# Performance work log

Measured on AMD Instinct MI355X. Metric: run time of the kernel, lower is better.

Reference implementation:

```python
import jax, jax.numpy as jnp
import numpy as np

N_NODES = 9
NEG_SLOPE = 0.2
# static edge list from the module (src, dst) pairs, PyG convention row0=src, row1=dst
_E = np.array([[0,1],[1,0],[0,3],[3,0],[0,5],[5,0],[0,7],[7,0],
               [1,2],[2,1],[3,4],[4,3],[5,6],[6,5],[7,8],[8,7]], dtype=np.int32).T
# GATv2Conv default add_self_loops=True
SRC = jnp.asarray(np.concatenate([_E[0], np.arange(N_NODES, dtype=np.int32)]))
DST = jnp.asarray(np.concatenate([_E[1], np.arange(N_NODES, dtype=np.int32)]))


def setup_inputs() -> dict:
    key = jax.random.key(0)
    k1, k2, k3, k4 = jax.random.split(key, 4)
    B, C_IN, C_OUT = 16384, 256, 256
    scale = 1.0 / np.sqrt(C_IN)
    return {
        "x": jax.random.normal(k1, (B, N_NODES, C_IN), jnp.float32),
        "W_l": jax.random.normal(k2, (C_IN, C_OUT), jnp.float32) * scale,
        "W_r": jax.random.normal(k3, (C_IN, C_OUT), jnp.float32) * scale,
        "att": jax.random.normal(k4, (C_OUT,), jnp.float32) * scale,
        "bias": jnp.zeros((C_OUT,), jnp.float32),
    }


def reference(x, W_l, W_r, att, bias):
    # x: [B, N, C_in] batch of identical small graphs
    xl = jnp.einsum("bnc,cd->bnd", x, W_l)  # source-side projection
    xr = jnp.einsum("bnc,cd->bnd", x, W_r)  # target-side projection
    # per-edge GATv2 score: a^T LeakyReLU(x_l[src] + x_r[dst])
    e = jax.nn.leaky_relu(xl[:, SRC] + xr[:, DST], NEG_SLOPE)  # [B, E, C_out]
    score = jnp.einsum("bed,d->be", e, att)                    # [B, E]
    # softmax over incoming edges of each destination node (segment softmax)
    sT = score.T                                               # [E, B]
    m = jax.ops.segment_max(sT, DST, num_segments=N_NODES)     # [N, B]
    ex = jnp.exp(sT - m[DST])
    denom = jax.ops.segment_sum(ex, DST, num_segments=N_NODES)
    alpha = ex / denom[DST]                                    # [E, B]
    # scatter-aggregate messages alpha * x_l[src] into dst
    msg = xl[:, SRC] * alpha.T[..., None]                      # [B, E, C_out]
    out = jax.ops.segment_sum(msg.transpose(1, 0, 2), DST, num_segments=N_NODES)
    return out.transpose(1, 0, 2) + bias                       # [B, N, C_out]
```

## Files before the change

### kernel.cpp

```cpp
#include <hip/hip_runtime.h>
#include <hip/hip_bf16.h>

typedef __attribute__((ext_vector_type(8))) short short8;
typedef __attribute__((ext_vector_type(4))) float f32x4;
typedef __attribute__((ext_vector_type(4))) unsigned short u16x4;

#define XLR_STRIDE 520
#define XLR_BYTES  (144 * XLR_STRIDE * 2)
#define LDS_BYTES  (XLR_BYTES + 1024 + 1600 + 1600)

__device__ __forceinline__ unsigned short f2bf(float f) {
    unsigned int u = __float_as_uint(f);
    unsigned int r = (u + 0x7fffu + ((u >> 16) & 1u)) >> 16;
    return (unsigned short)r;
}
__device__ __forceinline__ float bf2f(unsigned short h) {
    return __uint_as_float(((unsigned int)h) << 16);
}

__device__ const int SRC_E[25] = {0,1,0,3,0,5,0,7,1,2,3,4,5,6,7,8, 0,1,2,3,4,5,6,7,8};
__device__ const int DST_E[25] = {1,0,3,0,5,0,7,0,2,1,4,3,6,5,8,7, 0,1,2,3,4,5,6,7,8};
__device__ const int NINC[9]    = {5,3,2,3,2,3,2,3,2};
__device__ const int INC_OFF[9] = {0,5,8,10,13,15,18,20,23};
__device__ const int INC_E[25]  = {1,3,5,7,16, 0,9,17, 8,18, 2,11,19, 10,20, 4,13,21, 12,22, 6,15,23, 14,24};
__device__ const int INC_S[25]  = {1,3,5,7,0,  0,2,1,  1,2,  0,4,3,   3,4,   0,6,5,   5,6,   0,8,7,   7,8};

__global__ void convert_w_kernel(const float* __restrict__ Wl,
                                 const float* __restrict__ Wr,
                                 unsigned short* __restrict__ WT) {
    int n = blockIdx.x;
    int k = threadIdx.x;
    float v = (n < 256) ? Wl[k * 256 + n] : Wr[k * 256 + (n - 256)];
    WT[n * 256 + k] = f2bf(v);
}

__global__ __launch_bounds__(512, 2) void gat_fused_kernel(
        const float* __restrict__ x,
        const unsigned short* __restrict__ WT,
        const float* __restrict__ att,
        const float* __restrict__ bias,
        float* __restrict__ out) {
    __shared__ __align__(16) char smem[LDS_BYTES];
    unsigned short* XLR = (unsigned short*)smem;
    float* atts   = (float*)(smem + XLR_BYTES);
    float* scores = atts + 256;
    float* alphas = scores + 400;

    const int tid  = threadIdx.x;
    const int lane = tid & 63;
    const int wave = tid >> 6;
    const int blk  = blockIdx.x;

    if (tid < 256) atts[tid] = att[tid];

    const float* xblk = x + (size_t)blk * 36864;
    {
        f32x4 xv[18];
        #pragma unroll
        for (int it = 0; it < 18; ++it)
            xv[it] = *(const f32x4*)(xblk + it * 2048 + tid * 4);
        #pragma unroll
        for (int it = 0; it < 18; ++it) {
            int f   = it * 2048 + tid * 4;
            int row = f >> 8;
            int k   = f & 255;
            int inner = (k * 2) ^ ((row & 15) << 4);
            u16x4 w4 = { f2bf(xv[it][0]), f2bf(xv[it][1]), f2bf(xv[it][2]), f2bf(xv[it][3]) };
            *(u16x4*)(smem + row * 512 + inner) = w4;
        }
    }
    __syncthreads();

    const f32x4 ZERO = {0.f, 0.f, 0.f, 0.f};
    f32x4 acc[9][4];
    #pragma unroll
    for (int m = 0; m < 9; ++m)
        #pragma unroll
        for (int n = 0; n < 4; ++n) acc[m][n] = ZERO;

    const int nb = wave * 64;
    const unsigned short* Wbase = WT + (size_t)((nb + (lane & 15)) * 256 + ((lane >> 4) * 8));
    short8 bnx[4];
    #pragma unroll
    for (int n = 0; n < 4; ++n) bnx[n] = *(const short8*)(Wbase + n * 4096);

    #pragma unroll
    for (int kc = 0; kc < 8; ++kc) {
        short8 bn[4];
        #pragma unroll
        for (int n = 0; n < 4; ++n) bn[n] = bnx[n];
        if (kc < 7) {
            #pragma unroll
            for (int n = 0; n < 4; ++n)
                bnx[n] = *(const short8*)(Wbase + n * 4096 + (kc + 1) * 32);
        }
        short8 am[9];
        const int innerbase = ((kc * 64) + ((lane >> 4) * 16)) ^ ((lane & 15) << 4);
        #pragma unroll
        for (int m = 0; m < 9; ++m) {
            int row = m * 16 + (lane & 15);
            am[m] = *(const short8*)(smem + row * 512 + innerbase);
        }
        #pragma unroll
        for (int m = 0; m < 9; ++m)
            #pragma unroll
            for (int n = 0; n < 4; ++n)
                acc[m][n] = __builtin_amdgcn_mfma_f32_16x16x32_bf16(am[m], bn[n], acc[m][n], 0, 0, 0);
    }
    __syncthreads();

    #pragma unroll
    for (int m = 0; m < 9; ++m) {
        #pragma unroll
        for (int n = 0; n < 4; ++n) {
            int col = nb + n * 16 + (lane & 15);
            #pragma unroll
            for (int r = 0; r < 4; ++r) {
                int row = m * 16 + ((lane >> 4) * 4) + r;
                XLR[row * XLR_STRIDE + col] = f2bf(acc[m][n][r]);
            }
        }
    }
    __syncthreads();

    if (tid < 400) {
        int g = tid / 25, e = tid - g * 25;
        const unsigned short* pl = XLR + (g * 9 + SRC_E[e]) * XLR_STRIDE;
        const unsigned short* pr = XLR + (g * 9 + DST_E[e]) * XLR_STRIDE + 256;
        float s = 0.f;
        #pragma unroll 4
        for (int dc = 0; dc < 32; ++dc) {
            short8 a = *(const short8*)(pl + dc * 8);
            short8 b = *(const short8*)(pr + dc * 8);
            f32x4 at0 = *(const f32x4*)(atts + dc * 8);
            f32x4 at1 = *(const f32x4*)(atts + dc * 8 + 4);
            #pragma unroll
            for (int j = 0; j < 8; ++j) {
                float vv = bf2f((unsigned short)a[j]) + bf2f((unsigned short)b[j]);
                vv = vv > 0.f ? vv : 0.2f * vv;
                float aj = (j < 4) ? at0[j] : at1[j - 4];
                s += aj * vv;
            }
        }
        scores[tid] = s;
    }
    __syncthreads();

    if (tid < 144) {
        int g = tid / 9, n = tid - g * 9;
        int off = INC_OFF[n], cnt = NINC[n];
        float mx = -1e30f;
        for (int i = 0; i < cnt; ++i) mx = fmaxf(mx, scores[g * 25 + INC_E[off + i]]);
        float ssum = 0.f;
        for (int i = 0; i < cnt; ++i) ssum += __expf(scores[g * 25 + INC_E[off + i]] - mx);
        float inv = 1.f / ssum;
        for (int i = 0; i < cnt; ++i) {
            int e = INC_E[off + i];
            alphas[g * 25 + e] = __expf(scores[g * 25 + e] - mx) * inv;
        }
    }
    __syncthreads();

    const int d0 = lane * 4;
    f32x4 bv = *(const f32x4*)(bias + d0);
    float* outblk = out + (size_t)blk * 36864;
    for (int p = 0; p < 18; ++p) {
        int row = p * 8 + wave;
        int g = row / 9, n = row - g * 9;
        int off = INC_OFF[n], cnt = NINC[n];
        f32x4 v = bv;
        for (int i = 0; i < cnt; ++i) {
            float a = alphas[g * 25 + INC_E[off + i]];
            const unsigned short* pl = XLR + (g * 9 + INC_S[off + i]) * XLR_STRIDE + d0;
            u16x4 u = *(const u16x4*)pl;
            v[0] += a * bf2f(u[0]);
            v[1] += a * bf2f(u[1]);
            v[2] += a * bf2f(u[2]);
            v[3] += a * bf2f(u[3]);
        }
        *(f32x4*)(outblk + row * 256 + d0) = v;
    }
}

extern "C" void kernel_launch(void* const* d_in, const int* in_sizes, int n_in,
                              void* d_out, int out_size, void* d_ws, size_t ws_size,
                              hipStream_t stream) {
    const float* x    = (const float*)d_in[0];
    const float* Wl   = (const float*)d_in[1];
    const float* Wr   = (const float*)d_in[2];
    const float* att  = (const float*)d_in[3];
    const float* bias = (const float*)d_in[4];
    float* out = (float*)d_out;
    unsigned short* WT = (unsigned short*)d_ws;

    convert_w_kernel<<<512, 256, 0, stream>>>(Wl, Wr, WT);
    gat_fused_kernel<<<1024, 512, 0, stream>>>(x, WT, att, bias, out);
}
```

Before: 160.4 us.

## Keep projections in registers with node-major layout and compute scores from accumulators

The x tile is stored in shared memory node-major (row = node*16 + graph), so each MFMA M-tile holds a single node across 16 graphs. Each wave's column tiles now cover matching W_l and W_r columns. Edge scores and the final aggregation are computed straight from the fp32 MFMA accumulators, using cross-lane shuffles plus a small partials buffer, instead of writing bf16 xl/xr to LDS and reading them back. This removes the LDS round trip and one bf16 rounding of xl/xr, and shrinks LDS use, but output stores become strided scalar writes and accumulator register pressure goes up.

```diff
diff --git a/kernel.cpp b/kernel.cpp
--- a/kernel.cpp
+++ b/kernel.cpp
@@ -5,25 +5,26 @@
 typedef __attribute__((ext_vector_type(4))) float f32x4;
 typedef __attribute__((ext_vector_type(4))) unsigned short u16x4;
 
-#define XLR_STRIDE 520
-#define XLR_BYTES  (144 * XLR_STRIDE * 2)
-#define LDS_BYTES  (XLR_BYTES + 1024 + 1600 + 1600)
+#define STAGE_BYTES (144 * 512)
+#define PART_OFF    STAGE_BYTES
+#define ALPHA_OFF   (PART_OFF + 8 * 25 * 16 * 4)
+#define LDS_BYTES   (ALPHA_OFF + 25 * 16 * 4)
 
 __device__ __forceinline__ unsigned short f2bf(float f) {
     unsigned int u = __float_as_uint(f);
     unsigned int r = (u + 0x7fffu + ((u >> 16) & 1u)) >> 16;
     return (unsigned short)r;
 }
-__device__ __forceinline__ float bf2f(unsigned short h) {
-    return __uint_as_float(((unsigned int)h) << 16);
-}
-
-__device__ const int SRC_E[25] = {0,1,0,3,0,5,0,7,1,2,3,4,5,6,7,8, 0,1,2,3,4,5,6,7,8};
-__device__ const int DST_E[25] = {1,0,3,0,5,0,7,0,2,1,4,3,6,5,8,7, 0,1,2,3,4,5,6,7,8};
-__device__ const int NINC[9]    = {5,3,2,3,2,3,2,3,2};
-__device__ const int INC_OFF[9] = {0,5,8,10,13,15,18,20,23};
-__device__ const int INC_E[25]  = {1,3,5,7,16, 0,9,17, 8,18, 2,11,19, 10,20, 4,13,21, 12,22, 6,15,23, 14,24};
-__device__ const int INC_S[25]  = {1,3,5,7,0,  0,2,1,  1,2,  0,4,3,   3,4,   0,6,5,   5,6,   0,8,7,   7,8};
+
+constexpr int C_SRC[25] = {0,1,0,3,0,5,0,7,1,2,3,4,5,6,7,8, 0,1,2,3,4,5,6,7,8};
+constexpr int C_DST[25] = {1,0,3,0,5,0,7,0,2,1,4,3,6,5,8,7, 0,1,2,3,4,5,6,7,8};
+constexpr int C_NINC[9]  = {5,3,2,3,2,3,2,3,2};
+constexpr int C_IOFF[9]  = {0,5,8,10,13,15,18,20,23};
+constexpr int C_INCE[25] = {1,3,5,7,16, 0,9,17, 8,18, 2,11,19, 10,20, 4,13,21, 12,22, 6,15,23, 14,24};
+constexpr int C_INCS[25] = {1,3,5,7,0,  0,2,1,  1,2,  0,4,3,  3,4,  0,6,5,  5,6,  0,8,7,  7,8};
+__device__ const int D_NINC[9]  = {5,3,2,3,2,3,2,3,2};
+__device__ const int D_IOFF[9]  = {0,5,8,10,13,15,18,20,23};
+__device__ const int D_INCE[25] = {1,3,5,7,16, 0,9,17, 8,18, 2,11,19, 10,20, 4,13,21, 12,22, 6,15,23, 14,24};
 
 __global__ void convert_w_kernel(const float* __restrict__ Wl,
                                  const float* __restrict__ Wr,
@@ -41,17 +42,19 @@
         const float* __restrict__ bias,
         float* __restrict__ out) {
     __shared__ __align__(16) char smem[LDS_BYTES];
-    unsigned short* XLR = (unsigned short*)smem;
-    float* atts   = (float*)(smem + XLR_BYTES);
-    float* scores = atts + 256;
-    float* alphas = scores + 400;
+    float* partials = (float*)(smem + PART_OFF);
+    float* alphas   = (float*)(smem + ALPHA_OFF);
 
     const int tid  = threadIdx.x;
     const int lane = tid & 63;
-    const int wave = tid >> 6;
+    const int w    = tid >> 6;
+    const int gl   = lane >> 4;
+    const int li   = lane & 15;
     const int blk  = blockIdx.x;
 
-    if (tid < 256) atts[tid] = att[tid];
+    const int c0 = 32 * w + li, c1 = c0 + 16;
+    const float attc0 = att[c0], attc1 = att[c1];
+    const float bc0   = bias[c0], bc1 = bias[c1];
 
     const float* xblk = x + (size_t)blk * 36864;
     {
@@ -61,124 +64,123 @@
             xv[it] = *(const f32x4*)(xblk + it * 2048 + tid * 4);
         #pragma unroll
         for (int it = 0; it < 18; ++it) {
-            int f   = it * 2048 + tid * 4;
-            int row = f >> 8;
-            int k   = f & 255;
-            int inner = (k * 2) ^ ((row & 15) << 4);
-            u16x4 w4 = { f2bf(xv[it][0]), f2bf(xv[it][1]), f2bf(xv[it][2]), f2bf(xv[it][3]) };
-            *(u16x4*)(smem + row * 512 + inner) = w4;
+            int f    = it * 2048 + tid * 4;
+            int gr   = f >> 8;
+            int c    = f & 255;
+            int g    = gr / 9;
+            int node = gr - g * 9;
+            int srow = node * 16 + g;
+            u16x4 pk = { f2bf(xv[it][0]), f2bf(xv[it][1]), f2bf(xv[it][2]), f2bf(xv[it][3]) };
+            *(u16x4*)(smem + srow * 512 + ((2 * c) ^ (g << 4))) = pk;
         }
     }
     __syncthreads();
 
     const f32x4 ZERO = {0.f, 0.f, 0.f, 0.f};
-    f32x4 acc[9][4];
-    #pragma unroll
-    for (int m = 0; m < 9; ++m)
-        #pragma unroll
-        for (int n = 0; n < 4; ++n) acc[m][n] = ZERO;
-
-    const int nb = wave * 64;
-    const unsigned short* Wbase = WT + (size_t)((nb + (lane & 15)) * 256 + ((lane >> 4) * 8));
-    short8 bnx[4];
-    #pragma unroll
-    for (int n = 0; n < 4; ++n) bnx[n] = *(const short8*)(Wbase + n * 4096);
+    f32x4 aL[9][2], aR[9][2];
+    #pragma unroll
+    for (int m = 0; m < 9; ++m) {
+        aL[m][0] = ZERO; aL[m][1] = ZERO; aR[m][0] = ZERO; aR[m][1] = ZERO;
+    }
+    const unsigned short* WL0 = WT + (size_t)((32 * w + li) * 256 + gl * 8);
+    const unsigned short* WL1 = WL0 + 16 * 256;
+    const unsigned short* WR0 = WL0 + 256 * 256;
+    const unsigned short* WR1 = WR0 + 16 * 256;
 
     #pragma unroll
     for (int kc = 0; kc < 8; ++kc) {
-        short8 bn[4];
-        #pragma unroll
-        for (int n = 0; n < 4; ++n) bn[n] = bnx[n];
-        if (kc < 7) {
-            #pragma unroll
-            for (int n = 0; n < 4; ++n)
-                bnx[n] = *(const short8*)(Wbase + n * 4096 + (kc + 1) * 32);
-        }
+        short8 bl0 = *(const short8*)(WL0 + kc * 32);
+        short8 bl1 = *(const short8*)(WL1 + kc * 32);
+        short8 br0 = *(const short8*)(WR0 + kc * 32);
+        short8 br1 = *(const short8*)(WR1 + kc * 32);
+        const int inner = ((kc * 64) + (gl * 16)) ^ (li << 4);
         short8 am[9];
-        const int innerbase = ((kc * 64) + ((lane >> 4) * 16)) ^ ((lane & 15) << 4);
+        #pragma unroll
+        for (int m = 0; m < 9; ++m)
+            am[m] = *(const short8*)(smem + (m * 16 + li) * 512 + inner);
         #pragma unroll
         for (int m = 0; m < 9; ++m) {
-            int row = m * 16 + (lane & 15);
-            am[m] = *(const short8*)(smem + row * 512 + innerbase);
-        }
-        #pragma unroll
-        for (int m = 0; m < 9; ++m)
-            #pragma unroll
-            for (int n = 0; n < 4; ++n)
-                acc[m][n] = __builtin_amdgcn_mfma_f32_16x16x32_bf16(am[m], bn[n], acc[m][n], 0, 0, 0);
-    }
-    __syncthreads();
-
-    #pragma unroll
-    for (int m = 0; m < 9; ++m) {
-        #pragma unroll
-        for (int n = 0; n < 4; ++n) {
-            int col = nb + n * 16 + (lane & 15);
+            aL[m][0] = __builtin_amdgcn_mfma_f32_16x16x32_bf16(am[m], bl0, aL[m][0], 0, 0, 0);
+            aL[m][1] = __builtin_amdgcn_mfma_f32_16x16x32_bf16(am[m], bl1, aL[m][1], 0, 0, 0);
+            aR[m][0] = __builtin_amdgcn_mfma_f32_16x16x32_bf16(am[m], br0, aR[m][0], 0, 0, 0);
+            aR[m][1] = __builtin_amdgcn_mfma_f32_16x16x32_bf16(am[m], br1, aR[m][1], 0, 0, 0);
+        }
+    }
+
+    #pragma unroll
+    for (int e = 0; e < 25; ++e) {
+        const int s = C_SRC[e], d = C_DST[e];
+        float p0 = 0.f, p1 = 0.f, p2 = 0.f, p3 = 0.f;
+        #pragma unroll
+        for (int nt = 0; nt < 2; ++nt) {
+            const float ac = nt ? attc1 : attc0;
             #pragma unroll
             for (int r = 0; r < 4; ++r) {
-                int row = m * 16 + ((lane >> 4) * 4) + r;
-                XLR[row * XLR_STRIDE + col] = f2bf(acc[m][n][r]);
+                float v  = aL[s][nt][r] + aR[d][nt][r];
+                float lr = fmaxf(v, 0.2f * v);
+                float t  = ac * lr;
+                if (r == 0) p0 += t; else if (r == 1) p1 += t;
+                else if (r == 2) p2 += t; else p3 += t;
             }
         }
+        #pragma unroll
+        for (int m = 1; m < 16; m <<= 1) {
+            p0 += __shfl_xor(p0, m);
+            p1 += __shfl_xor(p1, m);
+            p2 += __shfl_xor(p2, m);
+            p3 += __shfl_xor(p3, m);
+        }
+        if (li == 0) {
+            f32x4 pk = {p0, p1, p2, p3};
+            *(f32x4*)(partials + (w * 25 + e) * 16 + 4 * gl) = pk;
+        }
     }
     __syncthreads();
 
-    if (tid < 400) {
-        int g = tid / 25, e = tid - g * 25;
-        const unsigned short* pl = XLR + (g * 9 + SRC_E[e]) * XLR_STRIDE;
-        const unsigned short* pr = XLR + (g * 9 + DST_E[e]) * XLR_STRIDE + 256;
-        float s = 0.f;
-        #pragma unroll 4
-        for (int dc = 0; dc < 32; ++dc) {
-            short8 a = *(const short8*)(pl + dc * 8);
-            short8 b = *(const short8*)(pr + dc * 8);
-            f32x4 at0 = *(const f32x4*)(atts + dc * 8);
-            f32x4 at1 = *(const f32x4*)(atts + dc * 8 + 4);
+    if (tid < 144) {
+        int n = tid >> 4, g = tid & 15;
+        int off = D_IOFF[n], cnt = D_NINC[n];
+        float mx = -1e30f;
+        for (int i = 0; i < cnt; ++i) {
+            int e = D_INCE[off + i];
+            float s = 0.f;
             #pragma unroll
-            for (int j = 0; j < 8; ++j) {
-                float vv = bf2f((unsigned short)a[j]) + bf2f((unsigned short)b[j]);
-                vv = vv > 0.f ? vv : 0.2f * vv;
-                float aj = (j < 4) ? at0[j] : at1[j - 4];
-                s += aj * vv;
-            }
-        }
-        scores[tid] = s;
-    }
-    __syncthreads();
-
-    if (tid < 144) {
-        int g = tid / 9, n = tid - g * 9;
-        int off = INC_OFF[n], cnt = NINC[n];
-        float mx = -1e30f;
-        for (int i = 0; i < cnt; ++i) mx = fmaxf(mx, scores[g * 25 + INC_E[off + i]]);
+            for (int ww = 0; ww < 8; ++ww) s += partials[(ww * 25 + e) * 16 + g];
+            alphas[e * 16 + g] = s;
+            mx = fmaxf(mx, s);
+        }
         float ssum = 0.f;
-        for (int i = 0; i < cnt; ++i) ssum += __expf(scores[g * 25 + INC_E[off + i]] - mx);
+        for (int i = 0; i < cnt; ++i)
+            ssum += __expf(alphas[D_INCE[off + i] * 16 + g] - mx);
         float inv = 1.f / ssum;
         for (int i = 0; i < cnt; ++i) {
-            int e = INC_E[off + i];
-            alphas[g * 25 + e] = __expf(scores[g * 25 + e] - mx) * inv;
+            int e = D_INCE[off + i];
+            alphas[e * 16 + g] = __expf(alphas[e * 16 + g] - mx) * inv;
         }
     }
     __syncthreads();
 
-    const int d0 = lane * 4;
-    f32x4 bv = *(const f32x4*)(bias + d0);
-    float* outblk = out + (size_t)blk * 36864;
-    for (int p = 0; p < 18; ++p) {
-        int row = p * 8 + wave;
-        int g = row / 9, n = row - g * 9;
-        int off = INC_OFF[n], cnt = NINC[n];
-        f32x4 v = bv;
-        for (int i = 0; i < cnt; ++i) {
-            float a = alphas[g * 25 + INC_E[off + i]];
-            const unsigned short* pl = XLR + (g * 9 + INC_S[off + i]) * XLR_STRIDE + d0;
-            u16x4 u = *(const u16x4*)pl;
-            v[0] += a * bf2f(u[0]);
-            v[1] += a * bf2f(u[1]);
-            v[2] += a * bf2f(u[2]);
-            v[3] += a * bf2f(u[3]);
-        }
-        *(f32x4*)(outblk + row * 256 + d0) = v;
+    #pragma unroll
+    for (int n = 0; n < 9; ++n) {
+        f32x4 o0 = {bc0, bc0, bc0, bc0};
+        f32x4 o1 = {bc1, bc1, bc1, bc1};
+        #pragma unroll
+        for (int i = 0; i < C_NINC[n]; ++i) {
+            const int e  = C_INCE[C_IOFF[n] + i];
+            const int sn = C_INCS[C_IOFF[n] + i];
+            f32x4 al = *(const f32x4*)(alphas + e * 16 + 4 * gl);
+            #pragma unroll
+            for (int r = 0; r < 4; ++r) {
+                o0[r] += al[r] * aL[sn][0][r];
+                o1[r] += al[r] * aL[sn][1][r];
+            }
+        }
+        #pragma unroll
+        for (int r = 0; r < 4; ++r) {
+            size_t row = (size_t)(blk * 16 + 4 * gl + r) * 9 + n;
+            out[row * 256 + c0] = o0[r];
+            out[row * 256 + c1] = o1[r];
+        }
     }
 }
 
```

Result: faster. 137.8 us (-14.1%).
